# Performance work log

Hardware: AMD Instinct MI355X
Metric: run time of the kernel (lower is better)

The kernel has to match this reference:

```python
import jax, jax.numpy as jnp
import numpy as np

SEQ, D, H = 4096, 1024, 16
HD = D // H
SCALE = HD ** -0.5


def setup_inputs() -> dict:
    key = jax.random.key(0)
    ks = jax.random.split(key, 8)
    s = 0.02
    return {
        "hidden_states": jax.random.normal(ks[0], (SEQ, D), dtype=jnp.float32),
        "wq": jax.random.normal(ks[1], (D, D), dtype=jnp.float32) * s,
        "bq": jax.random.normal(ks[2], (D,), dtype=jnp.float32) * s,
        "wk": jax.random.normal(ks[3], (D, D), dtype=jnp.float32) * s,
        "wv": jax.random.normal(ks[4], (D, D), dtype=jnp.float32) * s,
        "bv": jax.random.normal(ks[5], (D,), dtype=jnp.float32) * s,
        "wo": jax.random.normal(ks[6], (D, D), dtype=jnp.float32) * s,
        "bo": jax.random.normal(ks[7], (D,), dtype=jnp.float32) * s,
    }


def reference(hidden_states, wq, bq, wk, wv, bv, wo, bo):
    S = hidden_states.shape[0]
    # torch Linear: y = x @ W^T + b  (k_proj has no bias)
    q = (hidden_states @ wq.T + bq).reshape(S, H, HD).transpose(1, 0, 2)  # [H,S,hd]
    k = (hidden_states @ wk.T).reshape(S, H, HD).transpose(1, 0, 2)       # [H,S,hd]
    v = (hidden_states @ wv.T + bv).reshape(S, H, HD).transpose(1, 0, 2)  # [H,S,hd]
    scores = jnp.einsum('hqd,hkd->hqk', q, k) * SCALE                     # [H,S,S]
    # softmax computed in fp32 then cast back to query dtype
    attn = jax.nn.softmax(scores.astype(jnp.float32), axis=-1).astype(q.dtype)
    out = jnp.einsum('hqk,hkd->hqd', attn, v)                             # [H,S,hd]
    out = out.transpose(1, 0, 2).reshape(S, D)
    return out @ wo.T + bo
```

## Files before the change

### kernel.cpp

```cpp
#include <hip/hip_runtime.h>

#define SEQ 4096
#define DIM 1024
#define NH 16
#define HD 64
#define QKVSTR 3072

typedef __attribute__((ext_vector_type(8))) short bf16x8;
typedef __attribute__((ext_vector_type(4))) float f32x4;
typedef __attribute__((ext_vector_type(16))) float f32x16;
typedef __attribute__((ext_vector_type(4))) unsigned int uint4v;

__device__ __forceinline__ unsigned short f2bf(float f) {
  unsigned int b = __float_as_uint(f);
  b = b + 0x7fffu + ((b >> 16) & 1u);
  return (unsigned short)(b >> 16);
}

__device__ __forceinline__ unsigned int cvt_pk_bf16(float lo, float hi) {
  unsigned int r;
  asm("v_cvt_pk_bf16_f32 %0, %1, %2" : "=v"(r) : "v"(lo), "v"(hi));
  return r;
}

__device__ __forceinline__ float fast_exp2(float x) {
#if __has_builtin(__builtin_amdgcn_exp2f)
  return __builtin_amdgcn_exp2f(x);
#else
  float r; asm("v_exp_f32 %0, %1" : "=v"(r) : "v"(x)); return r;
#endif
}

typedef __attribute__((address_space(3))) unsigned int lds_uint;
typedef __attribute__((address_space(1))) const unsigned int global_uint;

__device__ __forceinline__ void gload_lds16(const void* g, void* l) {
  __builtin_amdgcn_global_load_lds((global_uint*)g, (lds_uint*)l, 16, 0, 0);
}

__global__ __launch_bounds__(256) void cast_all_kernel(
    const float* __restrict__ X, const float* __restrict__ wq, const float* __restrict__ wk,
    const float* __restrict__ wv, const float* __restrict__ wo,
    unsigned short* __restrict__ Xb, unsigned short* __restrict__ Wqkv,
    unsigned short* __restrict__ Wob, float qscale) {
  int i = blockIdx.x * 256 + threadIdx.x;
  const float* src;
  unsigned short* dst;
  float sc = 1.f;
  if (i < 524288) { src = X + (size_t)i * 8; dst = Xb + (size_t)i * 8; }
  else if (i < 655360) { int j = i - 524288; src = wq + (size_t)j * 8; dst = Wqkv + (size_t)j * 8; sc = qscale; }
  else if (i < 786432) { int j = i - 655360; src = wk + (size_t)j * 8; dst = Wqkv + 1048576 + (size_t)j * 8; }
  else if (i < 917504) { int j = i - 786432; src = wv + (size_t)j * 8; dst = Wqkv + 2097152 + (size_t)j * 8; }
  else { int j = i - 917504; src = wo + (size_t)j * 8; dst = Wob + (size_t)j * 8; }
  const float4* p = (const float4*)src;
  float4 x0 = p[0], x1 = p[1];
  union { unsigned short u[8]; uint4v v; } o;
  o.u[0] = f2bf(x0.x * sc); o.u[1] = f2bf(x0.y * sc);
  o.u[2] = f2bf(x0.z * sc); o.u[3] = f2bf(x0.w * sc);
  o.u[4] = f2bf(x1.x * sc); o.u[5] = f2bf(x1.y * sc);
  o.u[6] = f2bf(x1.z * sc); o.u[7] = f2bf(x1.w * sc);
  *(uint4v*)dst = o.v;
}

template<int BIASMODE, int OUT_F32>
__global__ __launch_bounds__(256) void gemm_bt_kernel(
    const unsigned short* __restrict__ A, const unsigned short* __restrict__ B,
    const float* __restrict__ b0, const float* __restrict__ b1, float qscale,
    void* __restrict__ Cout, int M, int N, int K) {
  __shared__ unsigned short As[128 * 32];
  __shared__ unsigned short Bs[128 * 32];
  int tid = threadIdx.x;
  int wave = tid >> 6, lane = tid & 63;
  int g = lane >> 4, lc = lane & 15;
  int wm = wave >> 1, wn = wave & 1;
  int m0 = blockIdx.y * 128, n0 = blockIdx.x * 128;

  f32x4 acc[4][4] = {};

  for (int k0 = 0; k0 < K; k0 += 32) {
    __syncthreads();
    for (int c = 0; c < 2; ++c) {
      int chunk = c * 256 + wave * 64 + lane;
      int row = chunk >> 2, cb = chunk & 3;
      gload_lds16(A + (size_t)(m0 + row) * K + k0 + cb * 8, As + (c * 256 + wave * 64) * 8);
      gload_lds16(B + (size_t)(n0 + row) * K + k0 + cb * 8, Bs + (c * 256 + wave * 64) * 8);
    }
    __syncthreads();
    bf16x8 af[4], bfr[4];
    for (int mf = 0; mf < 4; ++mf)
      af[mf] = *(const bf16x8*)&As[(wm * 64 + mf * 16 + lc) * 32 + g * 8];
    for (int nf = 0; nf < 4; ++nf)
      bfr[nf] = *(const bf16x8*)&Bs[(wn * 64 + nf * 16 + lc) * 32 + g * 8];
    for (int mf = 0; mf < 4; ++mf)
      for (int nf = 0; nf < 4; ++nf)
        acc[mf][nf] = __builtin_amdgcn_mfma_f32_16x16x32_bf16(af[mf], bfr[nf], acc[mf][nf], 0, 0, 0);
  }

  for (int nf = 0; nf < 4; ++nf) {
    int col = n0 + wn * 64 + nf * 16 + lc;
    float bias = 0.f;
    if (BIASMODE == 1) {
      int sect = col >> 10, cc = col & 1023;
      bias = (sect == 0) ? b0[cc] * qscale : ((sect == 2) ? b1[cc] : 0.f);
    } else if (BIASMODE == 2) {
      bias = b0[col];
    }
    for (int mf = 0; mf < 4; ++mf) {
      int row = m0 + wm * 64 + mf * 16 + g * 4;
      for (int r = 0; r < 4; ++r) {
        float v = acc[mf][nf][r] + bias;
        if (OUT_F32) ((float*)Cout)[(size_t)(row + r) * N + col] = v;
        else ((unsigned short*)Cout)[(size_t)(row + r) * N + col] = f2bf(v);
      }
    }
  }
}

__global__ __launch_bounds__(256) void transpose_kernel(
    const unsigned short* __restrict__ V, unsigned short* __restrict__ Vt) {
  __shared__ unsigned short Ts[64 * 72];
  int tid = threadIdx.x;
  int s0 = blockIdx.x * 64, d0 = blockIdx.y * 64;
  for (int c = 0; c < 2; ++c) {
    int q = c * 256 + tid;
    int r = q >> 3, cb = q & 7;
    uint4v v = *(const uint4v*)&V[(size_t)(s0 + r) * QKVSTR + d0 + cb * 8];
    *(uint4v*)&Ts[r * 72 + cb * 8] = v;
  }
  __syncthreads();
  for (int c = 0; c < 2; ++c) {
    int q = c * 256 + tid;
    int d = q >> 3, sc = q & 7;
    union { unsigned short u[8]; uint4v v; } ov;
    for (int j = 0; j < 8; ++j) ov.u[j] = Ts[(sc * 8 + j) * 72 + d];
    *(uint4v*)&Vt[(size_t)(d0 + d) * SEQ + s0 + sc * 8] = ov.v;
  }
}

__global__ __launch_bounds__(256) void attn_kernel(
    const unsigned short* __restrict__ QKV, const unsigned short* __restrict__ Vt,
    unsigned short* __restrict__ Aout) {
  __shared__ unsigned short Qs[128 * 64];
  __shared__ unsigned short Ks[2][64 * 64];
  __shared__ unsigned short Vs[2][64 * 64];
  int tid = threadIdx.x;
  int w = tid >> 6, lane = tid & 63;
  int hi = lane >> 5, l31 = lane & 31;

  int bid = blockIdx.x;
  int swz = (bid & 7) * 64 + (bid >> 3);
  int h = swz >> 5;
  int q0 = (swz & 31) * 128;

  const unsigned short* Qg = QKV + h * HD;
  const unsigned short* Kg = QKV + DIM + h * HD;
  const unsigned short* Vg = Vt + (size_t)(h * HD) * SEQ;

  int ch0 = w * 64 + lane;
  int r0s = ch0 >> 3, d0s = (ch0 & 7) ^ (r0s & 7);
  int ch1 = 256 + ch0;
  int r1s = ch1 >> 3, d1s = (ch1 & 7) ^ (r1s & 7);
  int koff0 = r0s * QKVSTR + d0s * 8;
  int koff1 = r1s * QKVSTR + d1s * 8;
  int voff0 = r0s * SEQ + d0s * 8;
  int voff1 = r1s * SEQ + d1s * 8;
  unsigned short* ldsK_lo[2] = { &Ks[0][(w * 64) * 8],       &Ks[1][(w * 64) * 8] };
  unsigned short* ldsK_hi[2] = { &Ks[0][(256 + w * 64) * 8], &Ks[1][(256 + w * 64) * 8] };
  unsigned short* ldsV_lo[2] = { &Vs[0][(w * 64) * 8],       &Vs[1][(w * 64) * 8] };
  unsigned short* ldsV_hi[2] = { &Vs[0][(256 + w * 64) * 8], &Vs[1][(256 + w * 64) * 8] };

  for (int c = 0; c < 4; ++c) {
    int chunk = c * 256 + w * 64 + lane;
    int row = chunk >> 3, pos = chunk & 7;
    int db = pos ^ (row & 7);
    gload_lds16(Qg + (size_t)(q0 + row) * QKVSTR + db * 8, Qs + (c * 256 + w * 64) * 8);
  }
  {
    const unsigned short* Kt = Kg;
    const unsigned short* Vtt = Vg;
    gload_lds16(Kt + koff0, ldsK_lo[0]);
    gload_lds16(Kt + koff1, ldsK_hi[0]);
    gload_lds16(Vtt + voff0, ldsV_lo[0]);
    gload_lds16(Vtt + voff1, ldsV_hi[0]);
  }
  asm volatile("s_waitcnt vmcnt(4)" ::: "memory");
  __builtin_amdgcn_sched_barrier(0);
  __builtin_amdgcn_s_barrier();

  bf16x8 qf[4];
  {
    int qrow = w * 32 + l31;
    for (int dc = 0; dc < 4; ++dc) {
      int pos = 2 * dc + hi;
      qf[dc] = *(const bf16x8*)&Qs[qrow * 64 + (pos ^ (qrow & 7)) * 8];
    }
  }

  f32x16 o0 = {}, o1 = {};
  float lsum = 0.f;
  int cur = 0;

  for (int t = 0; t < SEQ / 64; ++t) {
    {
      int kvn = ((t + 1) & (SEQ / 64 - 1)) * 64;
      const unsigned short* Kt = Kg + (size_t)kvn * QKVSTR;
      const unsigned short* Vtt = Vg + kvn;
      int nb = cur ^ 1;
      gload_lds16(Kt + koff0, ldsK_lo[nb]);
      gload_lds16(Kt + koff1, ldsK_hi[nb]);
      gload_lds16(Vtt + voff0, ldsV_lo[nb]);
      gload_lds16(Vtt + voff1, ldsV_hi[nb]);
    }
    asm volatile("s_waitcnt vmcnt(4)" ::: "memory");
    __builtin_amdgcn_sched_barrier(0);
    __builtin_amdgcn_s_barrier();
    __builtin_amdgcn_sched_barrier(0);

    bf16x8 kf[2][4];
    for (int f = 0; f < 2; ++f)
      for (int dc = 0; dc < 4; ++dc) {
        int krow = f * 32 + l31;
        int pos = 2 * dc + hi;
        kf[f][dc] = *(const bf16x8*)&Ks[cur][krow * 64 + (pos ^ (krow & 7)) * 8];
      }
    f32x16 st0 = {}, st1 = {};
    __builtin_amdgcn_s_setprio(1);
    for (int dc = 0; dc < 4; ++dc) {
      st0 = __builtin_amdgcn_mfma_f32_32x32x16_bf16(kf[0][dc], qf[dc], st0, 0, 0, 0);
      st1 = __builtin_amdgcn_mfma_f32_32x32x16_bf16(kf[1][dc], qf[dc], st1, 0, 0, 0);
    }
    __builtin_amdgcn_s_setprio(0);

    bf16x8 vf0[4], vf1[4];
#pragma unroll
    for (int c = 0; c < 4; ++c) {
      int pos = 2 * c + hi;
      int r0 = l31, r1 = 32 + l31;
      vf0[c] = *(const bf16x8*)&Vs[cur][r0 * 64 + (pos ^ (r0 & 7)) * 8];
      vf1[c] = *(const bf16x8*)&Vs[cur][r1 * 64 + (pos ^ (r1 & 7)) * 8];
    }

    float p0[16], p1[16];
    float ls = 0.f;
#pragma unroll
    for (int r = 0; r < 16; ++r) { p0[r] = fast_exp2(st0[r]); ls += p0[r]; }
#pragma unroll
    for (int r = 0; r < 16; ++r) { p1[r] = fast_exp2(st1[r]); ls += p1[r]; }
    lsum += ls;

    bf16x8 pa[4];
#pragma unroll
    for (int f = 0; f < 2; ++f) {
      const float* pp = f ? p1 : p0;
#pragma unroll
      for (int cc = 0; cc < 2; ++cc) {
        unsigned uLO0 = cvt_pk_bf16(pp[8 * cc + 0], pp[8 * cc + 1]);
        unsigned uLO1 = cvt_pk_bf16(pp[8 * cc + 2], pp[8 * cc + 3]);
        unsigned uHI0 = cvt_pk_bf16(pp[8 * cc + 4], pp[8 * cc + 5]);
        unsigned uHI1 = cvt_pk_bf16(pp[8 * cc + 6], pp[8 * cc + 7]);
        auto s0 = __builtin_amdgcn_permlane32_swap(uLO0, uHI0, false, false);
        auto s1 = __builtin_amdgcn_permlane32_swap(uLO1, uHI1, false, false);
        union { unsigned u[4]; bf16x8 v; } pw;
        pw.u[0] = s0[0]; pw.u[1] = s1[0]; pw.u[2] = s0[1]; pw.u[3] = s1[1];
        pa[f * 2 + cc] = pw.v;
      }
    }

    __builtin_amdgcn_s_setprio(1);
#pragma unroll
    for (int c = 0; c < 4; ++c) {
      o0 = __builtin_amdgcn_mfma_f32_32x32x16_bf16(pa[c], vf0[c], o0, 0, 0, 0);
      o1 = __builtin_amdgcn_mfma_f32_32x32x16_bf16(pa[c], vf1[c], o1, 0, 0, 0);
    }
    __builtin_amdgcn_s_setprio(0);

    asm volatile("" ::: "memory");
    __builtin_amdgcn_sched_barrier(0);
    __builtin_amdgcn_s_barrier();
    cur ^= 1;
  }

  lsum += __shfl_xor(lsum, 32);
  float inv = 1.f / lsum;
#pragma unroll
  for (int r = 0; r < 16; ++r) {
    int qr = (r & 3) + 8 * (r >> 2) + 4 * hi;
    float ir = __shfl(inv, qr + (lane & 32));
    size_t row = q0 + w * 32 + qr;
    Aout[row * DIM + h * HD + l31]      = f2bf(o0[r] * ir);
    Aout[row * DIM + h * HD + 32 + l31] = f2bf(o1[r] * ir);
  }
}

extern "C" void kernel_launch(void* const* d_in, const int* in_sizes, int n_in,
                              void* d_out, int out_size, void* d_ws, size_t ws_size,
                              hipStream_t stream) {
  (void)in_sizes; (void)n_in; (void)out_size; (void)ws_size;
  const float* X  = (const float*)d_in[0];
  const float* wq = (const float*)d_in[1];
  const float* bq = (const float*)d_in[2];
  const float* wk = (const float*)d_in[3];
  const float* wv = (const float*)d_in[4];
  const float* bv = (const float*)d_in[5];
  const float* wo = (const float*)d_in[6];
  const float* bo = (const float*)d_in[7];

  char* ws = (char*)d_ws;
  const size_t SZ_XD  = (size_t)SEQ * DIM * 2;
  const size_t SZ_W   = (size_t)DIM * DIM * 2;
  const size_t SZ_QKV = (size_t)SEQ * QKVSTR * 2;
  unsigned short* Xb   = (unsigned short*)(ws);
  unsigned short* Wqkv = (unsigned short*)(ws + SZ_XD);
  unsigned short* Wob  = (unsigned short*)(ws + SZ_XD + 3 * SZ_W);
  unsigned short* QKVb = (unsigned short*)(ws + SZ_XD + 4 * SZ_W);
  unsigned short* Vtb  = (unsigned short*)(ws + SZ_XD + 4 * SZ_W + SZ_QKV);
  unsigned short* Ab   = Xb;

  const float QSCALE = 0.125f * 1.44269504088896f;

  cast_all_kernel<<<4096, 256, 0, stream>>>(X, wq, wk, wv, wo, Xb, Wqkv, Wob, QSCALE);

  gemm_bt_kernel<1, 0><<<dim3(QKVSTR / 128, SEQ / 128), 256, 0, stream>>>(
      Xb, Wqkv, bq, bv, QSCALE, QKVb, SEQ, QKVSTR, DIM);

  transpose_kernel<<<dim3(SEQ / 64, DIM / 64), 256, 0, stream>>>(QKVb + 2 * DIM, Vtb);

  attn_kernel<<<SEQ / 128 * NH, 256, 0, stream>>>(QKVb, Vtb, Ab);

  gemm_bt_kernel<2, 1><<<dim3(DIM / 128, SEQ / 128), 256, 0, stream>>>(
      Ab, Wob, bo, nullptr, 1.f, d_out, SEQ, DIM, DIM);
}
```

Before: 170.8 us.

## Split attention KV range across two wave groups per block with LDS reduction

Doubles the attention block to 512 threads, with two groups of four waves each processing half of the key/value sequence for the same 128 queries, each group using its own double-buffered K/V LDS tiles. Partial outputs and row sums are combined through LDS at the end. The loop is also manually unrolled by two with precomputed LDS offsets, and the exp sum is split into four accumulators. This doubles the waves per block to hide latency, at the cost of more LDS per block and a final reduction step.

```diff
diff --git a/kernel.cpp b/kernel.cpp
--- a/kernel.cpp
+++ b/kernel.cpp
@@ -137,15 +137,16 @@
   }
 }
 
-__global__ __launch_bounds__(256) void attn_kernel(
+__global__ __launch_bounds__(512, 4) void attn_kernel(
     const unsigned short* __restrict__ QKV, const unsigned short* __restrict__ Vt,
     unsigned short* __restrict__ Aout) {
   __shared__ unsigned short Qs[128 * 64];
-  __shared__ unsigned short Ks[2][64 * 64];
-  __shared__ unsigned short Vs[2][64 * 64];
+  __shared__ unsigned short Ks[2][2][64 * 64];
+  __shared__ unsigned short Vs[2][2][64 * 64];
   int tid = threadIdx.x;
   int w = tid >> 6, lane = tid & 63;
   int hi = lane >> 5, l31 = lane & 31;
+  int qw = w & 3, grp = w >> 2;
 
   int bid = blockIdx.x;
   int swz = (bid & 7) * 64 + (bid >> 3);
@@ -155,33 +156,34 @@
   const unsigned short* Qg = QKV + h * HD;
   const unsigned short* Kg = QKV + DIM + h * HD;
   const unsigned short* Vg = Vt + (size_t)(h * HD) * SEQ;
-
-  int ch0 = w * 64 + lane;
+  int kvbase = grp * (SEQ / 2);
+
+  int ch0 = qw * 64 + lane;
   int r0s = ch0 >> 3, d0s = (ch0 & 7) ^ (r0s & 7);
   int ch1 = 256 + ch0;
   int r1s = ch1 >> 3, d1s = (ch1 & 7) ^ (r1s & 7);
-  int koff0 = r0s * QKVSTR + d0s * 8;
-  int koff1 = r1s * QKVSTR + d1s * 8;
-  int voff0 = r0s * SEQ + d0s * 8;
-  int voff1 = r1s * SEQ + d1s * 8;
-  unsigned short* ldsK_lo[2] = { &Ks[0][(w * 64) * 8],       &Ks[1][(w * 64) * 8] };
-  unsigned short* ldsK_hi[2] = { &Ks[0][(256 + w * 64) * 8], &Ks[1][(256 + w * 64) * 8] };
-  unsigned short* ldsV_lo[2] = { &Vs[0][(w * 64) * 8],       &Vs[1][(w * 64) * 8] };
-  unsigned short* ldsV_hi[2] = { &Vs[0][(256 + w * 64) * 8], &Vs[1][(256 + w * 64) * 8] };
-
-  for (int c = 0; c < 4; ++c) {
-    int chunk = c * 256 + w * 64 + lane;
+  size_t koff0 = (size_t)r0s * QKVSTR + d0s * 8;
+  size_t koff1 = (size_t)r1s * QKVSTR + d1s * 8;
+  size_t voff0 = (size_t)r0s * SEQ + d0s * 8;
+  size_t voff1 = (size_t)r1s * SEQ + d1s * 8;
+  unsigned short* sKlo[2] = { &Ks[grp][0][(qw * 64) * 8],       &Ks[grp][1][(qw * 64) * 8] };
+  unsigned short* sKhi[2] = { &Ks[grp][0][(256 + qw * 64) * 8], &Ks[grp][1][(256 + qw * 64) * 8] };
+  unsigned short* sVlo[2] = { &Vs[grp][0][(qw * 64) * 8],       &Vs[grp][1][(qw * 64) * 8] };
+  unsigned short* sVhi[2] = { &Vs[grp][0][(256 + qw * 64) * 8], &Vs[grp][1][(256 + qw * 64) * 8] };
+
+  for (int c = 0; c < 2; ++c) {
+    int chunk = c * 512 + w * 64 + lane;
     int row = chunk >> 3, pos = chunk & 7;
     int db = pos ^ (row & 7);
-    gload_lds16(Qg + (size_t)(q0 + row) * QKVSTR + db * 8, Qs + (c * 256 + w * 64) * 8);
+    gload_lds16(Qg + (size_t)(q0 + row) * QKVSTR + db * 8, Qs + (c * 512 + w * 64) * 8);
   }
   {
-    const unsigned short* Kt = Kg;
-    const unsigned short* Vtt = Vg;
-    gload_lds16(Kt + koff0, ldsK_lo[0]);
-    gload_lds16(Kt + koff1, ldsK_hi[0]);
-    gload_lds16(Vtt + voff0, ldsV_lo[0]);
-    gload_lds16(Vtt + voff1, ldsV_hi[0]);
+    const unsigned short* Kt = Kg + (size_t)kvbase * QKVSTR;
+    const unsigned short* Vtt = Vg + kvbase;
+    gload_lds16(Kt + koff0, sKlo[0]);
+    gload_lds16(Kt + koff1, sKhi[0]);
+    gload_lds16(Vtt + voff0, sVlo[0]);
+    gload_lds16(Vtt + voff1, sVhi[0]);
   }
   asm volatile("s_waitcnt vmcnt(4)" ::: "memory");
   __builtin_amdgcn_sched_barrier(0);
@@ -189,64 +191,76 @@
 
   bf16x8 qf[4];
   {
-    int qrow = w * 32 + l31;
+    int qrow = qw * 32 + l31;
     for (int dc = 0; dc < 4; ++dc) {
       int pos = 2 * dc + hi;
       qf[dc] = *(const bf16x8*)&Qs[qrow * 64 + (pos ^ (qrow & 7)) * 8];
     }
   }
 
+  int offb[4];
+#pragma unroll
+  for (int dc = 0; dc < 4; ++dc)
+    offb[dc] = l31 * 128 + (((2 * dc + hi) ^ (l31 & 7)) * 16);
+  const char* KbA = (const char*)&Ks[grp][0][0];
+  const char* KbB = (const char*)&Ks[grp][1][0];
+  const char* VbA = (const char*)&Vs[grp][0][0];
+  const char* VbB = (const char*)&Vs[grp][1][0];
+
   f32x16 o0 = {}, o1 = {};
-  float lsum = 0.f;
-  int cur = 0;
-
-  for (int t = 0; t < SEQ / 64; ++t) {
-    {
-      int kvn = ((t + 1) & (SEQ / 64 - 1)) * 64;
-      const unsigned short* Kt = Kg + (size_t)kvn * QKVSTR;
-      const unsigned short* Vtt = Vg + kvn;
-      int nb = cur ^ 1;
-      gload_lds16(Kt + koff0, ldsK_lo[nb]);
-      gload_lds16(Kt + koff1, ldsK_hi[nb]);
-      gload_lds16(Vtt + voff0, ldsV_lo[nb]);
-      gload_lds16(Vtt + voff1, ldsV_hi[nb]);
-    }
+  float la0 = 0.f, la1 = 0.f, la2 = 0.f, la3 = 0.f;
+
+  auto body = [&](int t, int CUR) {
+    int NB = CUR ^ 1;
+    int kvn = kvbase + (((t + 1) & 31) << 6);
+    const unsigned short* Kt = Kg + (size_t)kvn * QKVSTR;
+    const unsigned short* Vtt = Vg + kvn;
+    gload_lds16(Kt + koff0, sKlo[NB]);
+    gload_lds16(Kt + koff1, sKhi[NB]);
+    gload_lds16(Vtt + voff0, sVlo[NB]);
+    gload_lds16(Vtt + voff1, sVhi[NB]);
     asm volatile("s_waitcnt vmcnt(4)" ::: "memory");
     __builtin_amdgcn_sched_barrier(0);
     __builtin_amdgcn_s_barrier();
     __builtin_amdgcn_sched_barrier(0);
 
-    bf16x8 kf[2][4];
-    for (int f = 0; f < 2; ++f)
-      for (int dc = 0; dc < 4; ++dc) {
-        int krow = f * 32 + l31;
-        int pos = 2 * dc + hi;
-        kf[f][dc] = *(const bf16x8*)&Ks[cur][krow * 64 + (pos ^ (krow & 7)) * 8];
-      }
+    const char* Kb = CUR ? KbB : KbA;
+    const char* Vb = CUR ? VbB : VbA;
+    bf16x8 kf0[4], kf1[4];
+#pragma unroll
+    for (int dc = 0; dc < 4; ++dc) {
+      kf0[dc] = *(const bf16x8*)(Kb + offb[dc]);
+      kf1[dc] = *(const bf16x8*)(Kb + offb[dc] + 4096);
+    }
     f32x16 st0 = {}, st1 = {};
     __builtin_amdgcn_s_setprio(1);
+#pragma unroll
     for (int dc = 0; dc < 4; ++dc) {
-      st0 = __builtin_amdgcn_mfma_f32_32x32x16_bf16(kf[0][dc], qf[dc], st0, 0, 0, 0);
-      st1 = __builtin_amdgcn_mfma_f32_32x32x16_bf16(kf[1][dc], qf[dc], st1, 0, 0, 0);
+      st0 = __builtin_amdgcn_mfma_f32_32x32x16_bf16(kf0[dc], qf[dc], st0, 0, 0, 0);
+      st1 = __builtin_amdgcn_mfma_f32_32x32x16_bf16(kf1[dc], qf[dc], st1, 0, 0, 0);
     }
     __builtin_amdgcn_s_setprio(0);
 
     bf16x8 vf0[4], vf1[4];
 #pragma unroll
     for (int c = 0; c < 4; ++c) {
-      int pos = 2 * c + hi;
-      int r0 = l31, r1 = 32 + l31;
-      vf0[c] = *(const bf16x8*)&Vs[cur][r0 * 64 + (pos ^ (r0 & 7)) * 8];
-      vf1[c] = *(const bf16x8*)&Vs[cur][r1 * 64 + (pos ^ (r1 & 7)) * 8];
+      vf0[c] = *(const bf16x8*)(Vb + offb[c]);
+      vf1[c] = *(const bf16x8*)(Vb + offb[c] + 4096);
     }
 
     float p0[16], p1[16];
-    float ls = 0.f;
-#pragma unroll
-    for (int r = 0; r < 16; ++r) { p0[r] = fast_exp2(st0[r]); ls += p0[r]; }
-#pragma unroll
-    for (int r = 0; r < 16; ++r) { p1[r] = fast_exp2(st1[r]); ls += p1[r]; }
-    lsum += ls;
+#pragma unroll
+    for (int r = 0; r < 16; r += 4) {
+      p0[r] = fast_exp2(st0[r]); p0[r + 1] = fast_exp2(st0[r + 1]);
+      p0[r + 2] = fast_exp2(st0[r + 2]); p0[r + 3] = fast_exp2(st0[r + 3]);
+      la0 += p0[r]; la1 += p0[r + 1]; la2 += p0[r + 2]; la3 += p0[r + 3];
+    }
+#pragma unroll
+    for (int r = 0; r < 16; r += 4) {
+      p1[r] = fast_exp2(st1[r]); p1[r + 1] = fast_exp2(st1[r + 1]);
+      p1[r + 2] = fast_exp2(st1[r + 2]); p1[r + 3] = fast_exp2(st1[r + 3]);
+      la0 += p1[r]; la1 += p1[r + 1]; la2 += p1[r + 2]; la3 += p1[r + 3];
+    }
 
     bf16x8 pa[4];
 #pragma unroll
@@ -277,18 +291,47 @@
     asm volatile("" ::: "memory");
     __builtin_amdgcn_sched_barrier(0);
     __builtin_amdgcn_s_barrier();
-    cur ^= 1;
-  }
-
+  };
+
+  for (int tt = 0; tt < 32; tt += 2) {
+    body(tt + 0, 0);
+    body(tt + 1, 1);
+  }
+
+  float lsum = (la0 + la1) + (la2 + la3);
   lsum += __shfl_xor(lsum, 32);
-  float inv = 1.f / lsum;
-#pragma unroll
-  for (int r = 0; r < 16; ++r) {
-    int qr = (r & 3) + 8 * (r >> 2) + 4 * hi;
-    float ir = __shfl(inv, qr + (lane & 32));
-    size_t row = q0 + w * 32 + qr;
-    Aout[row * DIM + h * HD + l31]      = f2bf(o0[r] * ir);
-    Aout[row * DIM + h * HD + 32 + l31] = f2bf(o1[r] * ir);
+
+  __syncthreads();
+  float* cbO0 = (float*)&Ks[0][0][0];
+  float* cbO1 = (float*)&Vs[0][0][0];
+  float* cbL  = (float*)&Qs[0];
+  int cbase = (qw * 64 + lane) * 32;
+  int lx = lane & 31;
+  if (grp == 1) {
+#pragma unroll
+    for (int r = 0; r < 16; ++r) {
+      cbO0[cbase + (r ^ lx)] = o0[r];
+      cbO1[cbase + (r ^ lx)] = o1[r];
+    }
+    cbL[qw * 64 + lane] = lsum;
+  }
+  __syncthreads();
+  if (grp == 0) {
+#pragma unroll
+    for (int r = 0; r < 16; ++r) {
+      o0[r] += cbO0[cbase + (r ^ lx)];
+      o1[r] += cbO1[cbase + (r ^ lx)];
+    }
+    lsum += cbL[qw * 64 + lane];
+    float inv = 1.f / lsum;
+#pragma unroll
+    for (int r = 0; r < 16; ++r) {
+      int qr = (r & 3) + 8 * (r >> 2) + 4 * hi;
+      float ir = __shfl(inv, qr + (lane & 32));
+      size_t row = q0 + qw * 32 + qr;
+      Aout[row * DIM + h * HD + l31]      = f2bf(o0[r] * ir);
+      Aout[row * DIM + h * HD + 32 + l31] = f2bf(o1[r] * ir);
+    }
   }
 }
 
@@ -325,7 +368,7 @@
 
   transpose_kernel<<<dim3(SEQ / 64, DIM / 64), 256, 0, stream>>>(QKVb + 2 * DIM, Vtb);
 
-  attn_kernel<<<SEQ / 128 * NH, 256, 0, stream>>>(QKVb, Vtb, Ab);
+  attn_kernel<<<SEQ / 128 * NH, 512, 0, stream>>>(QKVb, Vtb, Ab);
 
   gemm_bt_kernel<2, 1><<<dim3(DIM / 128, SEQ / 128), 256, 0, stream>>>(
       Ab, Wob, bo, nullptr, 1.f, d_out, SEQ, DIM, DIM);
```

After: 298.1 us. 74.6% more time.

## Split attention KV range across two blocks and merge partials in combine kernel

Applied to the files above, without the earlier changes.

Each (head, query-tile) is split into two blocks that each process half of the key/value sequence, doubling the attention grid from 512 to 1024 blocks. This aims for better CU occupancy and latency hiding. Each half writes a normalized partial output plus its row sum, and a new combine kernel blends the two partials using the row-sum weights. The trade-off is an extra kernel launch and extra global traffic for the partial outputs and sums. The second partial reuses the already-consumed V region of the QKV buffer, and the sums reuse the QKV weight buffer.

```diff
diff --git a/kernel.cpp b/kernel.cpp
--- a/kernel.cpp
+++ b/kernel.cpp
@@ -139,7 +139,8 @@
 
 __global__ __launch_bounds__(256) void attn_kernel(
     const unsigned short* __restrict__ QKV, const unsigned short* __restrict__ Vt,
-    unsigned short* __restrict__ Aout) {
+    unsigned short* __restrict__ O0g, unsigned short* __restrict__ O1g,
+    float* __restrict__ Lg) {
   __shared__ unsigned short Qs[128 * 64];
   __shared__ unsigned short Ks[2][64 * 64];
   __shared__ unsigned short Vs[2][64 * 64];
@@ -148,9 +149,11 @@
   int hi = lane >> 5, l31 = lane & 31;
 
   int bid = blockIdx.x;
-  int swz = (bid & 7) * 64 + (bid >> 3);
-  int h = swz >> 5;
-  int q0 = (swz & 31) * 128;
+  int swz = (bid & 7) * 128 + (bid >> 3);
+  int h = swz >> 6;
+  int q0 = ((swz >> 1) & 31) * 128;
+  int hf = swz & 1;
+  int kvbase = hf * (SEQ / 2);
 
   const unsigned short* Qg = QKV + h * HD;
   const unsigned short* Kg = QKV + DIM + h * HD;
@@ -160,10 +163,10 @@
   int r0s = ch0 >> 3, d0s = (ch0 & 7) ^ (r0s & 7);
   int ch1 = 256 + ch0;
   int r1s = ch1 >> 3, d1s = (ch1 & 7) ^ (r1s & 7);
-  int koff0 = r0s * QKVSTR + d0s * 8;
-  int koff1 = r1s * QKVSTR + d1s * 8;
-  int voff0 = r0s * SEQ + d0s * 8;
-  int voff1 = r1s * SEQ + d1s * 8;
+  size_t koff0 = (size_t)r0s * QKVSTR + d0s * 8;
+  size_t koff1 = (size_t)r1s * QKVSTR + d1s * 8;
+  size_t voff0 = (size_t)r0s * SEQ + d0s * 8;
+  size_t voff1 = (size_t)r1s * SEQ + d1s * 8;
   unsigned short* ldsK_lo[2] = { &Ks[0][(w * 64) * 8],       &Ks[1][(w * 64) * 8] };
   unsigned short* ldsK_hi[2] = { &Ks[0][(256 + w * 64) * 8], &Ks[1][(256 + w * 64) * 8] };
   unsigned short* ldsV_lo[2] = { &Vs[0][(w * 64) * 8],       &Vs[1][(w * 64) * 8] };
@@ -176,8 +179,8 @@
     gload_lds16(Qg + (size_t)(q0 + row) * QKVSTR + db * 8, Qs + (c * 256 + w * 64) * 8);
   }
   {
-    const unsigned short* Kt = Kg;
-    const unsigned short* Vtt = Vg;
+    const unsigned short* Kt = Kg + (size_t)kvbase * QKVSTR;
+    const unsigned short* Vtt = Vg + kvbase;
     gload_lds16(Kt + koff0, ldsK_lo[0]);
     gload_lds16(Kt + koff1, ldsK_hi[0]);
     gload_lds16(Vtt + voff0, ldsV_lo[0]);
@@ -200,9 +203,9 @@
   float lsum = 0.f;
   int cur = 0;
 
-  for (int t = 0; t < SEQ / 64; ++t) {
+  for (int t = 0; t < 32; ++t) {
     {
-      int kvn = ((t + 1) & (SEQ / 64 - 1)) * 64;
+      int kvn = kvbase + (((t + 1) & 31) << 6);
       const unsigned short* Kt = Kg + (size_t)kvn * QKVSTR;
       const unsigned short* Vtt = Vg + kvn;
       int nb = cur ^ 1;
@@ -282,14 +285,40 @@
 
   lsum += __shfl_xor(lsum, 32);
   float inv = 1.f / lsum;
+  if (hi == 0)
+    Lg[(hf * NH + h) * SEQ + q0 + w * 32 + l31] = lsum;
+  unsigned short* Od = hf ? O1g : O0g;
+  int ostr = hf ? QKVSTR : DIM;
 #pragma unroll
   for (int r = 0; r < 16; ++r) {
     int qr = (r & 3) + 8 * (r >> 2) + 4 * hi;
     float ir = __shfl(inv, qr + (lane & 32));
     size_t row = q0 + w * 32 + qr;
-    Aout[row * DIM + h * HD + l31]      = f2bf(o0[r] * ir);
-    Aout[row * DIM + h * HD + 32 + l31] = f2bf(o1[r] * ir);
-  }
+    Od[row * ostr + h * HD + l31]      = f2bf(o0[r] * ir);
+    Od[row * ostr + h * HD + 32 + l31] = f2bf(o1[r] * ir);
+  }
+}
+
+__global__ __launch_bounds__(256) void combine_kernel(
+    unsigned short* __restrict__ A, const unsigned short* __restrict__ P1,
+    const float* __restrict__ L) {
+  int idx = blockIdx.x * 256 + threadIdx.x;
+  int row = idx >> 7, c8 = idx & 127;
+  int col = c8 << 3, h = col >> 6;
+  float l0 = L[h * SEQ + row];
+  float l1 = L[(NH + h) * SEQ + row];
+  float s = 1.f / (l0 + l1);
+  float w0 = l0 * s, w1 = l1 * s;
+  union { unsigned short u[8]; uint4v v; } a, b, o;
+  a.v = *(const uint4v*)&A[(size_t)row * DIM + col];
+  b.v = *(const uint4v*)&P1[(size_t)row * QKVSTR + col];
+#pragma unroll
+  for (int j = 0; j < 8; ++j) {
+    float fa = __uint_as_float((unsigned)(unsigned short)a.u[j] << 16);
+    float fb = __uint_as_float((unsigned)(unsigned short)b.u[j] << 16);
+    o.u[j] = f2bf(fa * w0 + fb * w1);
+  }
+  *(uint4v*)&A[(size_t)row * DIM + col] = o.v;
 }
 
 extern "C" void kernel_launch(void* const* d_in, const int* in_sizes, int n_in,
@@ -315,6 +344,7 @@
   unsigned short* QKVb = (unsigned short*)(ws + SZ_XD + 4 * SZ_W);
   unsigned short* Vtb  = (unsigned short*)(ws + SZ_XD + 4 * SZ_W + SZ_QKV);
   unsigned short* Ab   = Xb;
+  float*          Lg   = (float*)Wqkv;
 
   const float QSCALE = 0.125f * 1.44269504088896f;
 
@@ -325,7 +355,9 @@
 
   transpose_kernel<<<dim3(SEQ / 64, DIM / 64), 256, 0, stream>>>(QKVb + 2 * DIM, Vtb);
 
-  attn_kernel<<<SEQ / 128 * NH, 256, 0, stream>>>(QKVb, Vtb, Ab);
+  attn_kernel<<<SEQ / 128 * NH * 2, 256, 0, stream>>>(QKVb, Vtb, Ab, QKVb + 2 * DIM, Lg);
+
+  combine_kernel<<<SEQ * DIM / 8 / 256, 256, 0, stream>>>(Ab, QKVb + 2 * DIM, Lg);
 
   gemm_bt_kernel<2, 1><<<dim3(DIM / 128, SEQ / 128), 256, 0, stream>>>(
       Ab, Wob, bo, nullptr, 1.f, d_out, SEQ, DIM, DIM);
```

Result: slower. 175.8 us (+2.9%).

## Compute softmax row sums via MFMA with ones vector, precompute LDS offsets, swizzle GEMM tiles

Applied to the files above, without the earlier changes.

Replaces the per-lane VALU accumulation of exponentials with an extra MFMA multiplying the bf16 probabilities by a ones vector, moving row-sum work onto the matrix cores. The row sums are gathered through LDS at the end. Swizzled LDS read offsets are precomputed once outside the loop, and GEMM workgroup IDs are remapped in groups of 8 for better cache locality. This adds 4 MFMAs per tile, and the sums now use bf16-rounded probabilities, which slightly changes the normalisation.

```diff
diff --git a/kernel.cpp b/kernel.cpp
--- a/kernel.cpp
+++ b/kernel.cpp
@@ -73,7 +73,12 @@
   int wave = tid >> 6, lane = tid & 63;
   int g = lane >> 4, lc = lane & 15;
   int wm = wave >> 1, wn = wave & 1;
-  int m0 = blockIdx.y * 128, n0 = blockIdx.x * 128;
+
+  int gx = gridDim.x;
+  int wgid = blockIdx.y * gx + blockIdx.x;
+  int cpx = (gx * gridDim.y) >> 3;
+  int sw = (wgid & 7) * cpx + (wgid >> 3);
+  int m0 = (sw / gx) * 128, n0 = (sw % gx) * 128;
 
   f32x4 acc[4][4] = {};
 
@@ -160,10 +165,10 @@
   int r0s = ch0 >> 3, d0s = (ch0 & 7) ^ (r0s & 7);
   int ch1 = 256 + ch0;
   int r1s = ch1 >> 3, d1s = (ch1 & 7) ^ (r1s & 7);
-  int koff0 = r0s * QKVSTR + d0s * 8;
-  int koff1 = r1s * QKVSTR + d1s * 8;
-  int voff0 = r0s * SEQ + d0s * 8;
-  int voff1 = r1s * SEQ + d1s * 8;
+  size_t koff0 = (size_t)r0s * QKVSTR + d0s * 8;
+  size_t koff1 = (size_t)r1s * QKVSTR + d1s * 8;
+  size_t voff0 = (size_t)r0s * SEQ + d0s * 8;
+  size_t voff1 = (size_t)r1s * SEQ + d1s * 8;
   unsigned short* ldsK_lo[2] = { &Ks[0][(w * 64) * 8],       &Ks[1][(w * 64) * 8] };
   unsigned short* ldsK_hi[2] = { &Ks[0][(256 + w * 64) * 8], &Ks[1][(256 + w * 64) * 8] };
   unsigned short* ldsV_lo[2] = { &Vs[0][(w * 64) * 8],       &Vs[1][(w * 64) * 8] };
@@ -175,14 +180,10 @@
     int db = pos ^ (row & 7);
     gload_lds16(Qg + (size_t)(q0 + row) * QKVSTR + db * 8, Qs + (c * 256 + w * 64) * 8);
   }
-  {
-    const unsigned short* Kt = Kg;
-    const unsigned short* Vtt = Vg;
-    gload_lds16(Kt + koff0, ldsK_lo[0]);
-    gload_lds16(Kt + koff1, ldsK_hi[0]);
-    gload_lds16(Vtt + voff0, ldsV_lo[0]);
-    gload_lds16(Vtt + voff1, ldsV_hi[0]);
-  }
+  gload_lds16(Kg + koff0, ldsK_lo[0]);
+  gload_lds16(Kg + koff1, ldsK_hi[0]);
+  gload_lds16(Vg + voff0, ldsV_lo[0]);
+  gload_lds16(Vg + voff1, ldsV_hi[0]);
   asm volatile("s_waitcnt vmcnt(4)" ::: "memory");
   __builtin_amdgcn_sched_barrier(0);
   __builtin_amdgcn_s_barrier();
@@ -196,8 +197,20 @@
     }
   }
 
-  f32x16 o0 = {}, o1 = {};
-  float lsum = 0.f;
+  int offb[4];
+#pragma unroll
+  for (int dc = 0; dc < 4; ++dc)
+    offb[dc] = l31 * 128 + (((2 * dc + hi) ^ (l31 & 7)) * 16);
+  const char* KbA = (const char*)&Ks[0][0];
+  const char* KbB = (const char*)&Ks[1][0];
+  const char* VbA = (const char*)&Vs[0][0];
+  const char* VbB = (const char*)&Vs[1][0];
+
+  union { unsigned short us[8]; bf16x8 v; } one8;
+#pragma unroll
+  for (int j = 0; j < 8; ++j) one8.us[j] = 0x3F80;
+
+  f32x16 o0 = {}, o1 = {}, lsa = {};
   int cur = 0;
 
   for (int t = 0; t < SEQ / 64; ++t) {
@@ -216,37 +229,36 @@
     __builtin_amdgcn_s_barrier();
     __builtin_amdgcn_sched_barrier(0);
 
-    bf16x8 kf[2][4];
-    for (int f = 0; f < 2; ++f)
-      for (int dc = 0; dc < 4; ++dc) {
-        int krow = f * 32 + l31;
-        int pos = 2 * dc + hi;
-        kf[f][dc] = *(const bf16x8*)&Ks[cur][krow * 64 + (pos ^ (krow & 7)) * 8];
-      }
+    const char* Kb = cur ? KbB : KbA;
+    const char* Vb = cur ? VbB : VbA;
+
+    bf16x8 kf0[4], kf1[4];
+#pragma unroll
+    for (int dc = 0; dc < 4; ++dc) {
+      kf0[dc] = *(const bf16x8*)(Kb + offb[dc]);
+      kf1[dc] = *(const bf16x8*)(Kb + offb[dc] + 4096);
+    }
     f32x16 st0 = {}, st1 = {};
     __builtin_amdgcn_s_setprio(1);
+#pragma unroll
     for (int dc = 0; dc < 4; ++dc) {
-      st0 = __builtin_amdgcn_mfma_f32_32x32x16_bf16(kf[0][dc], qf[dc], st0, 0, 0, 0);
-      st1 = __builtin_amdgcn_mfma_f32_32x32x16_bf16(kf[1][dc], qf[dc], st1, 0, 0, 0);
+      st0 = __builtin_amdgcn_mfma_f32_32x32x16_bf16(kf0[dc], qf[dc], st0, 0, 0, 0);
+      st1 = __builtin_amdgcn_mfma_f32_32x32x16_bf16(kf1[dc], qf[dc], st1, 0, 0, 0);
     }
     __builtin_amdgcn_s_setprio(0);
 
     bf16x8 vf0[4], vf1[4];
 #pragma unroll
     for (int c = 0; c < 4; ++c) {
-      int pos = 2 * c + hi;
-      int r0 = l31, r1 = 32 + l31;
-      vf0[c] = *(const bf16x8*)&Vs[cur][r0 * 64 + (pos ^ (r0 & 7)) * 8];
-      vf1[c] = *(const bf16x8*)&Vs[cur][r1 * 64 + (pos ^ (r1 & 7)) * 8];
+      vf0[c] = *(const bf16x8*)(Vb + offb[c]);
+      vf1[c] = *(const bf16x8*)(Vb + offb[c] + 4096);
     }
 
     float p0[16], p1[16];
-    float ls = 0.f;
-#pragma unroll
-    for (int r = 0; r < 16; ++r) { p0[r] = fast_exp2(st0[r]); ls += p0[r]; }
-#pragma unroll
-    for (int r = 0; r < 16; ++r) { p1[r] = fast_exp2(st1[r]); ls += p1[r]; }
-    lsum += ls;
+#pragma unroll
+    for (int r = 0; r < 16; ++r) p0[r] = fast_exp2(st0[r]);
+#pragma unroll
+    for (int r = 0; r < 16; ++r) p1[r] = fast_exp2(st1[r]);
 
     bf16x8 pa[4];
 #pragma unroll
@@ -271,6 +283,7 @@
     for (int c = 0; c < 4; ++c) {
       o0 = __builtin_amdgcn_mfma_f32_32x32x16_bf16(pa[c], vf0[c], o0, 0, 0, 0);
       o1 = __builtin_amdgcn_mfma_f32_32x32x16_bf16(pa[c], vf1[c], o1, 0, 0, 0);
+      lsa = __builtin_amdgcn_mfma_f32_32x32x16_bf16(pa[c], one8.v, lsa, 0, 0, 0);
     }
     __builtin_amdgcn_s_setprio(0);
 
@@ -280,8 +293,13 @@
     cur ^= 1;
   }
 
-  lsum += __shfl_xor(lsum, 32);
-  float inv = 1.f / lsum;
+  float* Qf = (float*)Qs;
+  if (l31 == 0) {
+#pragma unroll
+    for (int r = 0; r < 16; ++r)
+      Qf[w * 32 + ((r & 3) + 8 * (r >> 2) + 4 * hi)] = lsa[r];
+  }
+  float inv = 1.f / Qf[w * 32 + l31];
 #pragma unroll
   for (int r = 0; r < 16; ++r) {
     int qr = (r & 3) + 8 * (r >> 2) + 4 * hi;
```

Result: no change. 170.0 us (-0.4%).
